# Optimization experiments

Measured on AMD Instinct MI355X. Metric: run time of the kernel, lower is better.

## Reference

```python
import jax, jax.numpy as jnp
import numpy as np

LEVELS = (1, 2, 4)
NHEAD = 4
LN_EPS = 1e-5


def _layernorm(x, g, b):
    m = jnp.mean(x, axis=-1, keepdims=True)
    v = jnp.mean((x - m) ** 2, axis=-1, keepdims=True)
    return (x - m) * jax.lax.rsqrt(v + LN_EPS) * g + b


def _spp_pool(x, starts, ends):
    # Exact AdaptiveAvgPool1d over per-proposal segments via inclusive-prefix-sum.
    # x: [B,C,T]; starts/ends: [B,P] int. Returns [B, P, C*sum(LEVELS)].
    B, C, T = x.shape
    P = starts.shape[1]
    xt = jnp.transpose(x, (0, 2, 1))  # [B,T,C]
    csum = jnp.concatenate([jnp.zeros((B, 1, C), x.dtype), jnp.cumsum(xt, axis=1)], axis=1)  # [B,T+1,C]
    n = ends - starts  # [B,P], always >= 1
    feats = []
    for L in LEVELS:
        i = jnp.arange(L)
        lo = (starts[..., None] + (i * n[..., None]) // L).reshape(B, P * L)
        hi = (starts[..., None] + ((i + 1) * n[..., None] + L - 1) // L).reshape(B, P * L)
        slo = jnp.take_along_axis(csum, lo[..., None], axis=1)  # [B,P*L,C]
        shi = jnp.take_along_axis(csum, hi[..., None], axis=1)
        mean = (shi - slo) / (hi - lo).astype(x.dtype)[..., None]
        # torch view(N, C*L) flattens [C,L] C-major -> transpose bins to last axis
        feats.append(mean.reshape(B, P, L, C).transpose(0, 1, 3, 2).reshape(B, P, C * L))
    return jnp.concatenate(feats, axis=-1)


def _encoder_layer(x, qkv_w, qkv_b, out_w, out_b, g1, b1, w1, bb1, w2, bb2, g2, b2):
    # Post-norm nn.TransformerEncoderLayer with exact-erf gelu, dropout=0 (eval)
    B, P, d = x.shape
    dh = d // NHEAD
    qkv = x @ qkv_w.T + qkv_b  # [B,P,3d]
    q, k, v = jnp.split(qkv, 3, axis=-1)
    sh = lambda t: t.reshape(B, P, NHEAD, dh).transpose(0, 2, 1, 3)  # [B,H,P,dh]
    q, k, v = sh(q), sh(k), sh(v)
    scale = 1.0 / float(np.sqrt(dh))
    attn = jax.nn.softmax(jnp.einsum('bhqd,bhkd->bhqk', q, k) * scale, axis=-1)
    o = jnp.einsum('bhqk,bhkd->bhqd', attn, v).transpose(0, 2, 1, 3).reshape(B, P, d)
    o = o @ out_w.T + out_b
    x = _layernorm(x + o, g1, b1)
    h = jax.nn.gelu(x @ w1.T + bb1, approximate=False) @ w2.T + bb2
    return _layernorm(x + h, g2, b2)


def _forward(x, proposal_boxes, proj_w, proj_b, pos_w1, pos_b1, pos_w2, pos_b2,
             qkv_w, qkv_b, out_w, out_b, ln1_g, ln1_b, ff1_w, ff1_b,
             ff2_w, ff2_b, ln2_g, ln2_b, cls_w, cls_b, det_w, det_b):
    B, C, T = x.shape
    P = proposal_boxes.shape[1]
    starts = jnp.clip(proposal_boxes[..., 0], 0, T - 1)
    ends = jnp.clip(proposal_boxes[..., 1], 1, T)
    ends = jnp.where(ends <= starts, jnp.minimum(starts + 1, T), ends)
    feats = _spp_pool(x, starts, ends)  # [B,P,spp_out_dim]
    s_f = proposal_boxes[..., 0].astype(x.dtype)
    e_f = proposal_boxes[..., 1].astype(x.dtype)
    centers = (s_f + e_f) / 2.0
    lengths = jnp.maximum(e_f - s_f, 1.0)
    pos_feat = jnp.stack([centers / T, lengths / T], axis=-1)  # [B,P,2]
    sort_idx = jnp.argsort(centers, axis=1)
    feats_s = jnp.take_along_axis(feats, sort_idx[..., None], axis=1)
    pos_emb = jax.nn.relu(pos_feat @ pos_w1.T + pos_b1) @ pos_w2.T + pos_b2
    pos_emb_s = jnp.take_along_axis(pos_emb, sort_idx[..., None], axis=1)
    tok = feats_s @ proj_w.T + proj_b + pos_emb_s  # [B,P,d]
    for l in range(qkv_w.shape[0]):
        tok = _encoder_layer(tok, qkv_w[l], qkv_b[l], out_w[l], out_b[l],
                             ln1_g[l], ln1_b[l], ff1_w[l], ff1_b[l],
                             ff2_w[l], ff2_b[l], ln2_g[l], ln2_b[l])
    inv = jnp.argsort(sort_idx, axis=1)
    ctx = jnp.take_along_axis(tok, inv[..., None], axis=1)  # [B,P,d]
    class_logits = ctx @ cls_w.T + cls_b  # [B,P,nc]
    det_logits = ctx @ det_w.T + det_b
    class_prob = jax.nn.softmax(class_logits, axis=2)
    det_prob = jax.nn.softmax(det_logits, axis=1)
    joint_prob = class_prob * det_prob
    video_prob = joint_prob.sum(axis=1)
    return video_prob, joint_prob, class_logits, det_logits, ctx


def setup_inputs() -> dict:
    key = jax.random.key(0)
    ks = jax.random.split(key, 32)
    B, C, T, P = 8, 512, 2048, 512
    d, dff, nc, nl = 512, 1024, 30, 2
    spp_out = C * sum(LEVELS)
    s = 0.02
    f32 = jnp.float32
    inp = {
        'x': jax.random.normal(ks[0], (B, C, T), f32),
        'proposal_boxes': jax.random.randint(ks[1], (B, P, 2), 0, T).astype(jnp.int32),
        'proj_w': jax.random.normal(ks[2], (d, spp_out), f32) * s,
        'proj_b': jnp.zeros((d,), f32),
        'pos_w1': jax.random.normal(ks[3], (d, 2), f32) * s,
        'pos_b1': jnp.zeros((d,), f32),
        'pos_w2': jax.random.normal(ks[4], (d, d), f32) * s,
        'pos_b2': jnp.zeros((d,), f32),
        'qkv_w': jax.random.normal(ks[5], (nl, 3 * d, d), f32) * s,
        'qkv_b': jnp.zeros((nl, 3 * d), f32),
        'out_w': jax.random.normal(ks[6], (nl, d, d), f32) * s,
        'out_b': jnp.zeros((nl, d), f32),
        'ln1_g': jnp.ones((nl, d), f32),
        'ln1_b': jnp.zeros((nl, d), f32),
        'ff1_w': jax.random.normal(ks[7], (nl, dff, d), f32) * s,
        'ff1_b': jnp.zeros((nl, dff), f32),
        'ff2_w': jax.random.normal(ks[8], (nl, d, dff), f32) * s,
        'ff2_b': jnp.zeros((nl, d), f32),
        'ln2_g': jnp.ones((nl, d), f32),
        'ln2_b': jnp.zeros((nl, d), f32),
        'cls_w': jax.random.normal(ks[9], (nc, d), f32) * s,
        'cls_b': jnp.zeros((nc,), f32),
        'det_w': jax.random.normal(ks[10], (nc, d), f32) * s,
        'det_b': jnp.zeros((nc,), f32),
    }
    return inp


def reference(x, proposal_boxes, proj_w, proj_b, pos_w1, pos_b1, pos_w2, pos_b2,
              qkv_w, qkv_b, out_w, out_b, ln1_g, ln1_b, ff1_w, ff1_b,
              ff2_w, ff2_b, ln2_g, ln2_b, cls_w, cls_b, det_w, det_b):
    return _forward(x, proposal_boxes, proj_w, proj_b, pos_w1, pos_b1, pos_w2, pos_b2,
                    qkv_w, qkv_b, out_w, out_b, ln1_g, ln1_b, ff1_w, ff1_b,
                    ff2_w, ff2_b, ln2_g, ln2_b, cls_w, cls_b, det_w, det_b)
```

## Files before the change

kernel.cpp:

```cpp
#include <hip/hip_runtime.h>

#define TDIM 2048
#define CDIM 512
#define BDIM 8
#define PDIM 512
#define DMODEL 512
#define NCOUT 30
#define SPPOUT 3584
#define AKDIM 4096

typedef __attribute__((ext_vector_type(8))) short short8;
typedef __attribute__((ext_vector_type(4))) short short4v;
typedef __attribute__((ext_vector_type(2))) short short2v;
typedef __attribute__((ext_vector_type(4))) float f32x4;

typedef const __attribute__((address_space(1))) void* as1cv;
typedef __attribute__((address_space(3))) void* as3v;

__device__ __forceinline__ void gl_lds16(const short* g, short* l){
  __builtin_amdgcn_global_load_lds((as1cv)g, (as3v)l, 16, 0, 0);
}

__device__ __forceinline__ short f2b(float f){
  unsigned u = __float_as_uint(f);
  unsigned r = (u + 0x7fffu + ((u >> 16) & 1u)) >> 16;
  return (short)r;
}

__device__ __forceinline__ float waveSum(float v){
#pragma unroll
  for (int o = 32; o > 0; o >>= 1) v += __shfl_xor(v, o);
  return v;
}
__device__ __forceinline__ float waveMax(float v){
#pragma unroll
  for (int o = 32; o > 0; o >>= 1) v = fmaxf(v, __shfl_xor(v, o));
  return v;
}

__global__ __launch_bounds__(512) void k0(
    const float* __restrict__ x, const int* __restrict__ boxes,
    const float* __restrict__ pw, const float* __restrict__ pw2,
    const float* __restrict__ qw, const float* __restrict__ ow,
    const float* __restrict__ f1, const float* __restrict__ f2,
    const float* __restrict__ cl, const float* __restrict__ dt,
    const float* __restrict__ pb, const float* __restrict__ pb2,
    const float* __restrict__ cb, const float* __restrict__ db,
    float* __restrict__ W, float* __restrict__ tot,
    int* __restrict__ sidx, float* __restrict__ out,
    short* __restrict__ Wc, short* __restrict__ Wd,
    float* __restrict__ bc, float* __restrict__ bh)
{
  __shared__ unsigned key[PDIM];
  int blk = blockIdx.x, t = threadIdx.x;
  if (blk < 256){
    int b = blk >> 5, ch = blk & 31;
    int c = t;
    const float* xp = x + ((size_t)(b * CDIM + c)) * TDIM + ch * 64;
    float* wp = W + ((size_t)b * TDIM + ch * 64) * CDIM + c;
    float run = 0.f;
    for (int tl = 0; tl < 64; tl += 4){
      float4 v = *(const float4*)(xp + tl);
      run += v.x; wp[(size_t)(tl + 0) * CDIM] = run;
      run += v.y; wp[(size_t)(tl + 1) * CDIM] = run;
      run += v.z; wp[(size_t)(tl + 2) * CDIM] = run;
      run += v.w; wp[(size_t)(tl + 3) * CDIM] = run;
    }
    tot[((size_t)b * 32 + ch) * CDIM + c] = run;
  } else if (blk < 264){
    int b = blk - 256;
    if (b == 0 && t < 240) out[t] = 0.f;
    int s = boxes[(size_t)(b * PDIM + t) * 2];
    int e = boxes[(size_t)(b * PDIM + t) * 2 + 1];
    key[t] = ((unsigned)(s + e) << 9) | (unsigned)t;
    __syncthreads();
    for (int k = 2; k <= PDIM; k <<= 1){
      for (int j = k >> 1; j > 0; j >>= 1){
        int ixj = t ^ j;
        if (ixj > t){
          unsigned a = key[t], c2 = key[ixj];
          bool up = ((t & k) == 0);
          bool doswap = up ? (a > c2) : (a < c2);
          if (doswap){ key[t] = c2; key[ixj] = a; }
        }
        __syncthreads();
      }
    }
    sidx[b * PDIM + t] = (int)(key[t] & 511u);
  } else {
    int i = (blk - 264) * 512 + t;
    if (i < 2097152){
      int r = i >> 12, k = i & 4095;
      float v = (k < SPPOUT) ? pw[(size_t)r * SPPOUT + k] : pw2[(size_t)r * DMODEL + (k - SPPOUT)];
      Wc[i] = f2b(v);
    } else if (i < 6322176){
      int j = i - 2097152;
      float v;
      if (j < 1572864) v = qw[j];
      else if (j < 2097152) v = ow[j - 1572864];
      else if (j < 3145728) v = f1[j - 2097152];
      else if (j < 4194304) v = f2[j - 3145728];
      else if (j < 4209664) v = cl[j - 4194304];
      else v = dt[j - 4209664];
      Wd[j] = f2b(v);
    } else {
      int k = i - 6322176;
      if (k < 512) bc[k] = pb[k] + pb2[k];
      else if (k < 572) bh[k - 512] = (k < 542) ? cb[k - 512] : db[k - 542];
    }
  }
}

__global__ void koff(const float* __restrict__ tot, float* __restrict__ off){
  int b = blockIdx.x >> 1, cg = blockIdx.x & 1;
  int c = cg * 256 + threadIdx.x;
  float run = 0.f;
  for (int ch = 0; ch < 32; ++ch){
    off[((size_t)b * 32 + ch) * CDIM + c] = run;
    run += tot[((size_t)b * 32 + ch) * CDIM + c];
  }
}

__global__ void kspp(const float* __restrict__ W, const float* __restrict__ off,
                     const int* __restrict__ boxes, const int* __restrict__ sidx,
                     const float* __restrict__ pw1, const float* __restrict__ pb1,
                     short* __restrict__ A){
  int blk = blockIdx.x;
  int b = blk >> 9, j = blk & 511;
  int p = sidx[b * PDIM + j];
  int s0 = boxes[(size_t)(b * PDIM + p) * 2];
  int e0 = boxes[(size_t)(b * PDIM + p) * 2 + 1];
  int start = min(max(s0, 0), TDIM - 1);
  int end   = min(max(e0, 1), TDIM);
  if (end <= start) end = min(start + 1, TDIM);
  int n = end - start;

  int lo[7], hi[7];
  {
    const int Ls[3] = {1, 2, 4};
    int q = 0;
    for (int li = 0; li < 3; ++li){
      int L = Ls[li];
      for (int i = 0; i < L; ++i){
        lo[q] = start + (i * n) / L;
        hi[q] = start + ((i + 1) * n + L - 1) / L;
        ++q;
      }
    }
  }
  float inv[7];
#pragma unroll
  for (int q = 0; q < 7; ++q) inv[q] = 1.f / (float)(hi[q] - lo[q]);

  int R[10] = { start - 1, end - 1, hi[1] - 1, lo[2] - 1, hi[3] - 1,
                lo[4] - 1, hi[4] - 1, lo[5] - 1, hi[5] - 1, lo[6] - 1 };

  float s_f = (float)s0, e_f = (float)e0;
  float px = (s_f + e_f) * 0.5f / (float)TDIM;
  float py = fmaxf(e_f - s_f, 1.f) / (float)TDIM;
  short* Ar = A + (size_t)(b * PDIM + j) * AKDIM;
  const float* Wb = W + (size_t)b * TDIM * CDIM;
  const float* ob = off + (size_t)b * 32 * CDIM;
#pragma unroll
  for (int cc = 0; cc < 2; ++cc){
    int c = threadIdx.x + cc * 256;
    float F[10];
#pragma unroll
    for (int u = 0; u < 10; ++u){
      int r = R[u];
      F[u] = (r < 0) ? 0.f : (Wb[(size_t)r * CDIM + c] + ob[(r >> 6) * CDIM + c]);
    }
    Ar[c]              = f2b((F[1] - F[0]) * inv[0]);
    Ar[512  + c * 2]   = f2b((F[2] - F[0]) * inv[1]);
    Ar[513  + c * 2]   = f2b((F[1] - F[3]) * inv[2]);
    Ar[1536 + c * 4]   = f2b((F[4] - F[0]) * inv[3]);
    Ar[1537 + c * 4]   = f2b((F[6] - F[5]) * inv[4]);
    Ar[1538 + c * 4]   = f2b((F[8] - F[7]) * inv[5]);
    Ar[1539 + c * 4]   = f2b((F[1] - F[9]) * inv[6]);
    float hv = pw1[c * 2] * px + pw1[c * 2 + 1] * py + pb1[c];
    Ar[SPPOUT + c] = f2b(fmaxf(hv, 0.f));
  }
}

template<int BN, int SWZ = 0>
__global__ __launch_bounds__(256) void gemm_bt(
    int M, int N, int K,
    const short* __restrict__ A, int lda, long long sAb, long long sAh,
    const short* __restrict__ B, int ldb, long long sBb, long long sBh,
    float* __restrict__ Cf, short* __restrict__ Cb, int ldc, long long sCb, long long sCh,
    int hdiv, float alpha,
    const float* __restrict__ bias, const float* __restrict__ resid, int act,
    short* __restrict__ Vtp)
{
  constexpr int JF = BN / 32;
  __shared__ short smem[128 * 64 + BN * 64];
  short* As = smem;
  short* Bs = smem + 128 * 64;
  int bx = blockIdx.x, by = blockIdx.y, bz = blockIdx.z;
  if constexpr (SWZ){
    int nx = gridDim.x, ny = gridDim.y;
    int rt = ny >> 3;
    int flat = (bz * ny + by) * nx + bx;
    int xcd = flat & 7, wl = flat >> 3;
    by = xcd * rt + wl % rt;
    int rest = wl / rt;
    bx = rest % nx;
    bz = rest / nx;
  }
  int zb = bz / hdiv, zh = bz - zb * hdiv;
  A += (size_t)zb * sAb + (size_t)zh * sAh;
  B += (size_t)zb * sBb + (size_t)zh * sBh;
  size_t coff = (size_t)zb * sCb + (size_t)zh * sCh;
  int rowBase = by * 128, colBase = bx * BN;
  int t = threadIdx.x;
  int lane = t & 63;
  int wave = t >> 6;
  int wm = (wave >> 1) * 64, wn = (wave & 1) * (BN / 2);
  int lm = lane & 15, quad = lane >> 4;
  int srow = t >> 3;
  int skw = ((t & 7) * 8) ^ ((srow & 7) * 8);

  const short* Agp[4];
#pragma unroll
  for (int it = 0; it < 4; ++it)
    Agp[it] = A + (size_t)min(rowBase + srow + it * 32, M - 1) * lda + skw;
  const short* Bgp[JF];
#pragma unroll
  for (int it = 0; it < JF; ++it)
    Bgp[it] = B + (size_t)min(colBase + srow + it * 32, N - 1) * ldb + skw;

  f32x4 zero4 = {0.f, 0.f, 0.f, 0.f};
  f32x4 acc[4][JF];
#pragma unroll
  for (int i = 0; i < 4; ++i)
#pragma unroll
    for (int j = 0; j < JF; ++j) acc[i][j] = zero4;

  int axr = (lm & 7) * 8;
  for (int k0 = 0; k0 < K; k0 += 64){
#pragma unroll
    for (int it = 0; it < 4; ++it) gl_lds16(Agp[it] + k0, As + it * 2048 + t * 8);
#pragma unroll
    for (int it = 0; it < JF; ++it) gl_lds16(Bgp[it] + k0, Bs + it * 2048 + t * 8);
    __syncthreads();
#pragma unroll
    for (int h = 0; h < 2; ++h){
      int koff = (h * 32 + quad * 8) ^ axr;
      short8 af[4], bfr[JF];
#pragma unroll
      for (int i = 0; i < 4; ++i)
        af[i] = *(const short8*)(As + (wm + i * 16 + lm) * 64 + koff);
#pragma unroll
      for (int j = 0; j < JF; ++j)
        bfr[j] = *(const short8*)(Bs + (wn + j * 16 + lm) * 64 + koff);
#pragma unroll
      for (int i = 0; i < 4; ++i)
#pragma unroll
        for (int j = 0; j < JF; ++j)
          acc[i][j] = __builtin_amdgcn_mfma_f32_16x16x32_bf16(af[i], bfr[j], acc[i][j], 0, 0, 0);
    }
    __syncthreads();
  }

  if (Vtp && colBase >= 1024){
    short* LT = smem;
#pragma unroll
    for (int i = 0; i < 4; ++i){
#pragma unroll
      for (int j = 0; j < JF; ++j){
        int d = wn + j * 16 + lm;
        int prow = wm + i * 16 + quad * 4;
        short4v pk;
#pragma unroll
        for (int r = 0; r < 4; ++r){
          float v = acc[i][j][r] * alpha;
          if (bias) v += bias[colBase + d];
          pk[r] = f2b(v);
        }
        *(short4v*)(LT + d * 132 + prow) = pk;
      }
    }
    __syncthreads();
    int bb = rowBase >> 9;
    int hh = (colBase - 1024) >> 7;
    int dd0 = (colBase - 1024) & 127;
    int dl = t >> 2, pl = (t & 3) * 32;
    const short* sp = LT + dl * 132 + pl;
    short* dp = Vtp + ((size_t)(bb * 4 + hh)) * 65536 + (size_t)(dd0 + dl) * 512 + (rowBase & 511) + pl;
#pragma unroll
    for (int u = 0; u < 4; ++u) *(short8*)(dp + u * 8) = *(const short8*)(sp + u * 8);
    return;
  }

#pragma unroll
  for (int i = 0; i < 4; ++i){
#pragma unroll
    for (int j = 0; j < JF; ++j){
#pragma unroll
      for (int r = 0; r < 4; ++r){
        int row = rowBase + wm + i * 16 + quad * 4 + r;
        int col = colBase + wn + j * 16 + lm;
        if (row < M && col < N){
          float v = acc[i][j][r] * alpha;
          if (bias) v += bias[col];
          size_t ci = coff + (size_t)row * ldc + col;
          if (resid) v += resid[ci];
          if (act) v = 0.5f * v * (1.f + erff(v * 0.7071067811865476f));
          if (Cf) Cf[ci] = v;
          if (Cb) Cb[ci] = f2b(v);
        }
      }
    }
  }
}

__global__ void kredG1(const float* __restrict__ part, const float* __restrict__ bias,
                       float* __restrict__ tok, short* __restrict__ tokb){
  int idx = blockIdx.x * 256 + threadIdx.x;
  const float4* p = (const float4*)part;
  float4 v0 = p[idx], v1 = p[idx + 524288], v2 = p[idx + 1048576], v3 = p[idx + 1572864];
  float4 bv = ((const float4*)bias)[idx & 127];
  float4 v;
  v.x = v0.x + v1.x + v2.x + v3.x + bv.x;
  v.y = v0.y + v1.y + v2.y + v3.y + bv.y;
  v.z = v0.z + v1.z + v2.z + v3.z + bv.z;
  v.w = v0.w + v1.w + v2.w + v3.w + bv.w;
  ((float4*)tok)[idx] = v;
  short4v s4 = { f2b(v.x), f2b(v.y), f2b(v.z), f2b(v.w) };
  *(short4v*)(tokb + (size_t)idx * 4) = s4;
}

__global__ __launch_bounds__(256) void kflash(const short* __restrict__ qkvb,
                                              const short* __restrict__ Vt,
                                              short* __restrict__ ob){
  __shared__ float Ofs[4][16][128];
  __shared__ float Ml[4][16], Ll[4][16], Fw[4][16], Linv[16];
  int bid = blockIdx.x;
  int bh = bid & 31, qt = bid >> 5;
  int b = bh >> 2, h = bh & 3;
  int t = threadIdx.x;
  int w = t >> 6, lane = t & 63;
  int lm = lane & 15, quad = lane >> 4;
  const float SL2 = 0.1275174468f;

  const short* qbase = qkvb + (size_t)(b * 512 + qt * 16 + lm) * 1536 + h * 128 + quad * 8;
  short8 qf[4];
#pragma unroll
  for (int s = 0; s < 4; ++s) qf[s] = *(const short8*)(qbase + s * 32);

  const short* kbase = qkvb + (size_t)(b * 512) * 1536 + 512 + h * 128 + quad * 8;
  const short* vbase = Vt + (size_t)bh * 65536 + (size_t)lm * 512 + quad * 8;

  f32x4 zero4 = {0.f, 0.f, 0.f, 0.f};
  f32x4 Of[8];
#pragma unroll
  for (int i = 0; i < 8; ++i) Of[i] = zero4;
  float mrun[4] = {-1e30f, -1e30f, -1e30f, -1e30f};
  float lrun[4] = {0.f, 0.f, 0.f, 0.f};
  short* Pw = (short*)&Ofs[w][0][0];

#pragma unroll
  for (int kt = 0; kt < 2; ++kt){
    int kb = w * 128 + kt * 64;
    f32x4 Sf[4];
#pragma unroll
    for (int j = 0; j < 4; ++j) Sf[j] = zero4;
#pragma unroll
    for (int s = 0; s < 4; ++s){
#pragma unroll
      for (int j = 0; j < 4; ++j){
        short8 kf = *(const short8*)(kbase + (size_t)(kb + j * 16 + lm) * 1536 + s * 32);
        Sf[j] = __builtin_amdgcn_mfma_f32_16x16x32_bf16(qf[s], kf, Sf[j], 0, 0, 0);
      }
    }
    float alpha[4];
#pragma unroll
    for (int r = 0; r < 4; ++r){
      float mx = fmaxf(fmaxf(Sf[0][r], Sf[1][r]), fmaxf(Sf[2][r], Sf[3][r])) * SL2;
#pragma unroll
      for (int o = 1; o < 16; o <<= 1) mx = fmaxf(mx, __shfl_xor(mx, o));
      float mnew = fmaxf(mrun[r], mx);
      alpha[r] = exp2f(mrun[r] - mnew);
      float psum = 0.f;
#pragma unroll
      for (int j = 0; j < 4; ++j){
        float p = exp2f(Sf[j][r] * SL2 - mnew);
        Sf[j][r] = p;
        psum += p;
      }
#pragma unroll
      for (int o = 1; o < 16; o <<= 1) psum += __shfl_xor(psum, o);
      lrun[r] = lrun[r] * alpha[r] + psum;
      mrun[r] = mnew;
    }
#pragma unroll
    for (int i = 0; i < 8; ++i)
#pragma unroll
      for (int r = 0; r < 4; ++r) Of[i][r] *= alpha[r];
#pragma unroll
    for (int j = 0; j < 4; ++j)
#pragma unroll
      for (int r = 0; r < 4; ++r){
        int q = quad * 4 + r;
        int key = j * 16 + lm;
        Pw[q * 64 + (key ^ ((q & 7) * 8))] = f2b(Sf[j][r]);
      }
#pragma unroll
    for (int ts = 0; ts < 2; ++ts){
      short8 pa = *(const short8*)(Pw + lm * 64 + (((ts * 32 + quad * 8) ^ ((lm & 7) * 8))));
#pragma unroll
      for (int jd = 0; jd < 8; ++jd){
        short8 vf = *(const short8*)(vbase + (size_t)(jd * 16) * 512 + kb + ts * 32);
        Of[jd] = __builtin_amdgcn_mfma_f32_16x16x32_bf16(pa, vf, Of[jd], 0, 0, 0);
      }
    }
  }

#pragma unroll
  for (int jd = 0; jd < 8; ++jd)
#pragma unroll
    for (int r = 0; r < 4; ++r)
      Ofs[w][quad * 4 + r][jd * 16 + lm] = Of[jd][r];
  if (lm == 0){
#pragma unroll
    for (int r = 0; r < 4; ++r){
      Ml[w][quad * 4 + r] = mrun[r];
      Ll[w][quad * 4 + r] = lrun[r];
    }
  }
  __syncthreads();

  if (t < 64){
    int wv = t >> 4, row = t & 15;
    float M = fmaxf(fmaxf(Ml[0][row], Ml[1][row]), fmaxf(Ml[2][row], Ml[3][row]));
    Fw[wv][row] = exp2f(Ml[wv][row] - M);
    if (wv == 0){
      float lsum = Ll[0][row] * exp2f(Ml[0][row] - M) + Ll[1][row] * exp2f(Ml[1][row] - M)
                 + Ll[2][row] * exp2f(Ml[2][row] - M) + Ll[3][row] * exp2f(Ml[3][row] - M);
      Linv[row] = 1.f / lsum;
    }
  }
  __syncthreads();

  {
    int row = t >> 4, dbase = (t & 15) * 8;
    float f0 = Fw[0][row], f1 = Fw[1][row], f2v = Fw[2][row], f3 = Fw[3][row];
    float li = Linv[row];
    short* dst = ob + ((size_t)(b * 512 + qt * 16 + row)) * 512 + h * 128 + dbase;
#pragma unroll
    for (int u = 0; u < 8; ++u){
      float v = Ofs[0][row][dbase + u] * f0 + Ofs[1][row][dbase + u] * f1
              + Ofs[2][row][dbase + u] * f2v + Ofs[3][row][dbase + u] * f3;
      dst[u] = f2b(v * li);
    }
  }
}

__global__ __launch_bounds__(256) void klnR(const float* __restrict__ part,
                     const float* __restrict__ bias,
                     const float* __restrict__ resid,
                     const float* __restrict__ g, const float* __restrict__ bb,
                     float* __restrict__ Yf, short* __restrict__ Yb){
  int row = blockIdx.x * 4 + (threadIdx.x >> 6), lane = threadIdx.x & 63;
  size_t base = (size_t)row * DMODEL;
  float v[8]; float s = 0.f;
#pragma unroll
  for (int i = 0; i < 8; ++i){
    int c = lane + 64 * i;
    v[i] = part[base + c] + part[base + c + 2097152] + bias[c] + resid[base + c];
    s += v[i];
  }
  s = waveSum(s);
  float m = s * (1.f / DMODEL);
  float q = 0.f;
#pragma unroll
  for (int i = 0; i < 8; ++i){ float d = v[i] - m; q += d * d; }
  q = waveSum(q);
  float inv = rsqrtf(q * (1.f / DMODEL) + 1e-5f);
#pragma unroll
  for (int i = 0; i < 8; ++i){
    int c = lane + 64 * i;
    float o = (v[i] - m) * inv * g[c] + bb[c];
    Yf[base + c] = o;
    Yb[base + c] = f2b(o);
  }
}

__global__ void kdetsm(const float* __restrict__ hd, float* __restrict__ dp){
  int b = blockIdx.x / NCOUT, c = blockIdx.x % NCOUT, lane = threadIdx.x;
  float v[8]; float m = -1e30f;
#pragma unroll
  for (int i = 0; i < 8; ++i){
    v[i] = hd[((size_t)(b * PDIM) + lane + 64 * i) * 60 + 30 + c];
    m = fmaxf(m, v[i]);
  }
  m = waveMax(m);
  float s = 0.f;
#pragma unroll
  for (int i = 0; i < 8; ++i){ s += expf(v[i] - m); }
  s = waveSum(s);
  if (lane == 0){
    dp[b * NCOUT + c] = m;
    dp[240 + b * NCOUT + c] = 1.f / s;
  }
}

__global__ __launch_bounds__(256) void kfinal(const float* __restrict__ hd,
                       const float* __restrict__ dps,
                       const float* __restrict__ tok, const int* __restrict__ sidx,
                       float* __restrict__ out){
  int blk = blockIdx.x * 4 + (threadIdx.x >> 6);
  int b = blk >> 9, j = blk & 511;
  int lane = threadIdx.x & 63;
  int p = sidx[b * PDIM + j];
  float* video = out;
  float* joint = out + 240;
  float* clso  = out + 123120;
  float* deto  = out + 246000;
  float* ctxo  = out + 368880;
  size_t rs60 = (size_t)(b * PDIM + j) * 60;
  size_t ro = (size_t)(b * PDIM + p) * NCOUT;
  float lc = (lane < NCOUT) ? hd[rs60 + lane] : -1e30f;
  float m = waveMax(lc);
  float e = (lane < NCOUT) ? expf(lc - m) : 0.f;
  float s = waveSum(e);
  float cp = e / s;
  if (lane < NCOUT){
    float dv  = hd[rs60 + 30 + lane];
    float dpv = expf(dv - dps[b * NCOUT + lane]) * dps[240 + b * NCOUT + lane];
    float jp  = cp * dpv;
    clso[ro + lane] = lc;
    deto[ro + lane] = dv;
    joint[ro + lane] = jp;
    atomicAdd(&video[b * NCOUT + lane], jp);
  }
  const float4* tr = (const float4*)(tok + (size_t)(b * PDIM + j) * DMODEL);
  float4* cr = (float4*)(ctxo + (size_t)(b * PDIM + p) * DMODEL);
  for (int c = lane; c < DMODEL / 4; c += 64) cr[c] = tr[c];
}

extern "C" void kernel_launch(void* const* d_in, const int* in_sizes, int n_in,
                              void* d_out, int out_size, void* d_ws, size_t ws_size,
                              hipStream_t stream) {
  const float* x      = (const float*)d_in[0];
  const int*   boxes  = (const int*)d_in[1];
  const float* proj_w = (const float*)d_in[2];
  const float* proj_b = (const float*)d_in[3];
  const float* pos_w1 = (const float*)d_in[4];
  const float* pos_b1 = (const float*)d_in[5];
  const float* pos_w2 = (const float*)d_in[6];
  const float* pos_b2 = (const float*)d_in[7];
  const float* qkv_w  = (const float*)d_in[8];
  const float* qkv_b  = (const float*)d_in[9];
  const float* out_w  = (const float*)d_in[10];
  const float* out_b  = (const float*)d_in[11];
  const float* ln1_g  = (const float*)d_in[12];
  const float* ln1_b  = (const float*)d_in[13];
  const float* ff1_w  = (const float*)d_in[14];
  const float* ff1_b  = (const float*)d_in[15];
  const float* ff2_w  = (const float*)d_in[16];
  const float* ff2_b  = (const float*)d_in[17];
  const float* ln2_g  = (const float*)d_in[18];
  const float* ln2_b  = (const float*)d_in[19];
  const float* cls_w  = (const float*)d_in[20];
  const float* cls_b  = (const float*)d_in[21];
  const float* det_w  = (const float*)d_in[22];
  const float* det_b  = (const float*)d_in[23];
  float* out = (float*)d_out;
  float* ws  = (float*)d_ws;

  const size_t oR1    = 0;
  const size_t oS     = 9437184;
  const size_t oOff   = 17825792;
  const size_t oTok   = 22020096;
  const size_t oTokb  = 24117248;
  const size_t oTok2  = 25165824;
  const size_t oTok2b = 27262976;
  const size_t oWcat  = 28311552;
  const size_t oBcat  = 29360128;
  const size_t oWq    = 29360640;
  const size_t oWo    = 30147072;
  const size_t oWf1   = 30409216;
  const size_t oWf2   = 30933504;
  const size_t oWcls  = 31457792;
  const size_t oTot   = 31473152;
  const size_t oBhead = 31604224;
  const size_t oSidx  = 31608320;

  short* Abf   = (short*)(ws + oR1);
  short* qkvb  = (short*)(ws + oR1);
  short* Vt    = (short*)(ws + oR1 + 3145728);
  short* obufb = (short*)(ws + oR1 + 4194304);
  short* hbufb = (short*)(ws + oR1 + 5242880);
  float* headS = ws + oR1 + 7340032;
  float* dpS   = ws + oR1 + 7585792;
  float* csum  = ws + oS;
  float* Cpart = ws + oS;
  float* Cp2   = ws + oS;
  float* offp  = ws + oOff;
  float* tok   = ws + oTok;
  short* tokb  = (short*)(ws + oTokb);
  float* tok2  = ws + oTok2;
  short* tok2b = (short*)(ws + oTok2b);
  short* Wcatb = (short*)(ws + oWcat);
  float* bcat  = ws + oBcat;
  short* Wq    = (short*)(ws + oWq);
  short* Wo    = (short*)(ws + oWo);
  short* Wf1   = (short*)(ws + oWf1);
  short* Wf2   = (short*)(ws + oWf2);
  short* Whead = (short*)(ws + oWcls);
  float* tot   = ws + oTot;
  float* bhead = ws + oBhead;
  int*   sidx  = (int*)(ws + oSidx);

  k0<<<12614, 512, 0, stream>>>(x, boxes, proj_w, pos_w2, qkv_w, out_w, ff1_w, ff2_w,
                                cls_w, det_w, proj_b, pos_b2, cls_b, det_b,
                                csum, tot, sidx, out, Wcatb, Wq, bcat, bhead);
  koff<<<16, 256, 0, stream>>>(tot, offp);
  kspp<<<BDIM * PDIM, 256, 0, stream>>>(csum, offp, boxes, sidx, pos_w1, pos_b1, Abf);

  gemm_bt<64, 1><<<dim3(8, 32, 4), 256, 0, stream>>>(
      4096, 512, 1024, Abf, 4096, 1024, 0, Wcatb, 4096, 1024, 0,
      Cpart, nullptr, 512, 2097152, 0, 1, 1.f, nullptr, nullptr, 0, nullptr);
  kredG1<<<2048, 256, 0, stream>>>(Cpart, bcat, tok, tokb);

  for (int l = 0; l < 2; ++l){
    const short* qw  = Wq  + (size_t)l * 1536 * 512;
    const short* ow  = Wo  + (size_t)l * 512 * 512;
    const short* f1w = Wf1 + (size_t)l * 1024 * 512;
    const short* f2w = Wf2 + (size_t)l * 512 * 1024;
    const float* qb  = qkv_b + (size_t)l * 1536;
    const float* obv = out_b + (size_t)l * 512;
    const float* f1b = ff1_b + (size_t)l * 1024;
    const float* f2b_ = ff2_b + (size_t)l * 512;

    gemm_bt<64><<<dim3(24, 32, 1), 256, 0, stream>>>(
        4096, 1536, 512, tokb, 512, 0, 0, qw, 512, 0, 0,
        nullptr, qkvb, 1536, 0, 0, 1, 1.f, qb, nullptr, 0, Vt);
    kflash<<<1024, 256, 0, stream>>>(qkvb, Vt, obufb);
    gemm_bt<64><<<dim3(8, 32, 2), 256, 0, stream>>>(
        4096, 512, 256, obufb, 512, 256, 0, ow, 512, 256, 0,
        Cp2, nullptr, 512, 2097152, 0, 1, 1.f, nullptr, nullptr, 0, nullptr);
    klnR<<<1024, 256, 0, stream>>>(Cp2, obv, tok, ln1_g + l * 512, ln1_b + l * 512, tok2, tok2b);
    gemm_bt<64><<<dim3(16, 32, 1), 256, 0, stream>>>(
        4096, 1024, 512, tok2b, 512, 0, 0, f1w, 512, 0, 0,
        nullptr, hbufb, 1024, 0, 0, 1, 1.f, f1b, nullptr, 1, nullptr);
    gemm_bt<64><<<dim3(8, 32, 2), 256, 0, stream>>>(
        4096, 512, 512, hbufb, 1024, 512, 0, f2w, 1024, 512, 0,
        Cp2, nullptr, 512, 2097152, 0, 1, 1.f, nullptr, nullptr, 0, nullptr);
    klnR<<<1024, 256, 0, stream>>>(Cp2, f2b_, tok2, ln2_g + l * 512, ln2_b + l * 512, tok, tokb);
  }

  gemm_bt<64><<<dim3(1, 32, 1), 256, 0, stream>>>(
      4096, 60, 512, tokb, 512, 0, 0, Whead, 512, 0, 0,
      headS, nullptr, 60, 0, 0, 1, 1.f, bhead, nullptr, 0, nullptr);
  kdetsm<<<BDIM * NCOUT, 64, 0, stream>>>(headS, dpS);
  kfinal<<<1024, 256, 0, stream>>>(headS, dpS, tok, sidx, out);
}
```

Measured before the change: 480.6 us.

## Vectorize weight bf16 conversion and fuse head GEMM with detection softmax stats

```diff
diff --git a/kernel.cpp b/kernel.cpp
--- a/kernel.cpp
+++ b/kernel.cpp
@@ -25,6 +25,9 @@
   unsigned u = __float_as_uint(f);
   unsigned r = (u + 0x7fffu + ((u >> 16) & 1u)) >> 16;
   return (short)r;
+}
+__device__ __forceinline__ float b2f(unsigned short u){
+  return __uint_as_float(((unsigned)u) << 16);
 }
 
 __device__ __forceinline__ float waveSum(float v){
@@ -88,25 +91,35 @@
     }
     sidx[b * PDIM + t] = (int)(key[t] & 511u);
   } else {
-    int i = (blk - 264) * 512 + t;
-    if (i < 2097152){
-      int r = i >> 12, k = i & 4095;
-      float v = (k < SPPOUT) ? pw[(size_t)r * SPPOUT + k] : pw2[(size_t)r * DMODEL + (k - SPPOUT)];
-      Wc[i] = f2b(v);
-    } else if (i < 6322176){
-      int j = i - 2097152;
-      float v;
-      if (j < 1572864) v = qw[j];
-      else if (j < 2097152) v = ow[j - 1572864];
-      else if (j < 3145728) v = f1[j - 2097152];
-      else if (j < 4194304) v = f2[j - 3145728];
-      else if (j < 4209664) v = cl[j - 4194304];
-      else v = dt[j - 4209664];
-      Wd[j] = f2b(v);
-    } else {
-      int k = i - 6322176;
-      if (k < 512) bc[k] = pb[k] + pb2[k];
-      else if (k < 572) bh[k - 512] = (k < 542) ? cb[k - 512] : db[k - 542];
+    int i4 = (blk - 264) * 512 + t;
+    if (i4 < 524288){
+      int base = i4 * 4;
+      int r = base >> 12, k = base & 4095;
+      float4 v;
+      if (k < SPPOUT) v = *(const float4*)(pw + (size_t)r * SPPOUT + k);
+      else            v = *(const float4*)(pw2 + (size_t)r * DMODEL + (k - SPPOUT));
+      short4v s = { f2b(v.x), f2b(v.y), f2b(v.z), f2b(v.w) };
+      *(short4v*)(Wc + base) = s;
+    } else if (i4 < 1580544){
+      int j = i4 * 4 - 2097152;
+      const float* src; int off;
+      if (j < 1572864){ src = qw; off = j; }
+      else if (j < 2097152){ src = ow; off = j - 1572864; }
+      else if (j < 3145728){ src = f1; off = j - 2097152; }
+      else if (j < 4194304){ src = f2; off = j - 3145728; }
+      else if (j < 4209664){ src = cl; off = j - 4194304; }
+      else { src = dt; off = j - 4209664; }
+      float4 v = *(const float4*)(src + off);
+      short4v s = { f2b(v.x), f2b(v.y), f2b(v.z), f2b(v.w) };
+      *(short4v*)(Wd + j) = s;
+    } else if (i4 < 1580688){
+      int k = (i4 - 1580544) * 4;
+#pragma unroll
+      for (int u = 0; u < 4; ++u){
+        int kk = k + u;
+        if (kk < 512) bc[kk] = pb[kk] + pb2[kk];
+        else if (kk < 572) bh[kk - 512] = (kk < 542) ? cb[kk - 512] : db[kk - 542];
+      }
     }
   }
 }
@@ -486,22 +499,53 @@
   }
 }
 
-__global__ void kdetsm(const float* __restrict__ hd, float* __restrict__ dp){
-  int b = blockIdx.x / NCOUT, c = blockIdx.x % NCOUT, lane = threadIdx.x;
-  float v[8]; float m = -1e30f;
-#pragma unroll
-  for (int i = 0; i < 8; ++i){
-    v[i] = hd[((size_t)(b * PDIM) + lane + 64 * i) * 60 + 30 + c];
-    m = fmaxf(m, v[i]);
-  }
-  m = waveMax(m);
-  float s = 0.f;
-#pragma unroll
-  for (int i = 0; i < 8; ++i){ s += expf(v[i] - m); }
-  s = waveSum(s);
-  if (lane == 0){
-    dp[b * NCOUT + c] = m;
-    dp[240 + b * NCOUT + c] = 1.f / s;
+__global__ __launch_bounds__(256) void kheadcol(const short* __restrict__ tokb,
+                                                const short* __restrict__ Whead,
+                                                const float* __restrict__ bhead,
+                                                float* __restrict__ headS,
+                                                float* __restrict__ dp){
+  __shared__ float wf[512];
+  __shared__ float redM[4], redS[4];
+  int b = blockIdx.x / 60, col = blockIdx.x % 60;
+  int t = threadIdx.x;
+  {
+    short2v wv = *(const short2v*)(Whead + col * 512 + t * 2);
+    wf[t * 2]     = b2f((unsigned short)wv[0]);
+    wf[t * 2 + 1] = b2f((unsigned short)wv[1]);
+  }
+  __syncthreads();
+  float bias = bhead[col];
+  float val[2];
+#pragma unroll
+  for (int rr = 0; rr < 2; ++rr){
+    int r = t + rr * 256;
+    const short* row = tokb + ((size_t)(b * 512 + r)) * 512;
+    float acc = 0.f;
+#pragma unroll 8
+    for (int k = 0; k < 512; k += 8){
+      short8 v = *(const short8*)(row + k);
+#pragma unroll
+      for (int u = 0; u < 8; ++u) acc += b2f((unsigned short)v[u]) * wf[k + u];
+    }
+    val[rr] = acc + bias;
+    headS[(size_t)(b * 512 + r) * 60 + col] = val[rr];
+  }
+  if (col >= 30){
+    int lane = t & 63, w = t >> 6;
+    float mx = fmaxf(val[0], val[1]);
+    mx = waveMax(mx);
+    if (lane == 0) redM[w] = mx;
+    __syncthreads();
+    float M = fmaxf(fmaxf(redM[0], redM[1]), fmaxf(redM[2], redM[3]));
+    float se = expf(val[0] - M) + expf(val[1] - M);
+    se = waveSum(se);
+    if (lane == 0) redS[w] = se;
+    __syncthreads();
+    if (t == 0){
+      float S = redS[0] + redS[1] + redS[2] + redS[3];
+      dp[b * NCOUT + (col - 30)] = M;
+      dp[240 + b * NCOUT + (col - 30)] = 1.f / S;
+    }
   }
 }
 
@@ -613,9 +657,9 @@
   float* bhead = ws + oBhead;
   int*   sidx  = (int*)(ws + oSidx);
 
-  k0<<<12614, 512, 0, stream>>>(x, boxes, proj_w, pos_w2, qkv_w, out_w, ff1_w, ff2_w,
-                                cls_w, det_w, proj_b, pos_b2, cls_b, det_b,
-                                csum, tot, sidx, out, Wcatb, Wq, bcat, bhead);
+  k0<<<3352, 512, 0, stream>>>(x, boxes, proj_w, pos_w2, qkv_w, out_w, ff1_w, ff2_w,
+                               cls_w, det_w, proj_b, pos_b2, cls_b, det_b,
+                               csum, tot, sidx, out, Wcatb, Wq, bcat, bhead);
   koff<<<16, 256, 0, stream>>>(tot, offp);
   kspp<<<BDIM * PDIM, 256, 0, stream>>>(csum, offp, boxes, sidx, pos_w1, pos_b1, Abf);
 
@@ -651,9 +695,6 @@
     klnR<<<1024, 256, 0, stream>>>(Cp2, f2b_, tok2, ln2_g + l * 512, ln2_b + l * 512, tok, tokb);
   }
 
-  gemm_bt<64><<<dim3(1, 32, 1), 256, 0, stream>>>(
-      4096, 60, 512, tokb, 512, 0, 0, Whead, 512, 0, 0,
-      headS, nullptr, 60, 0, 0, 1, 1.f, bhead, nullptr, 0, nullptr);
-  kdetsm<<<BDIM * NCOUT, 64, 0, stream>>>(headS, dpS);
+  kheadcol<<<480, 256, 0, stream>>>(tokb, Whead, bhead, headS, dpS);
   kfinal<<<1024, 256, 0, stream>>>(headS, dpS, tok, sidx, out);
 }
```

Result: slower. 504.2 us (+4.9%).
